# Kernel tuning notes

Measured on AMD Instinct MI355X. Metric: run time of the kernel, lower is better.

## Reference

```python
import jax, jax.numpy as jnp
import numpy as np

N = 8192
D = 512
INSTANCES = 8  # samples per class (balanced PK batch)
ALPHA = 40.0
BASE = 0.5
BIG = 1e9  # finite sentinel instead of inf (safe under vjp)


def setup_inputs() -> dict:
    key = jax.random.key(0)
    emb = jax.random.normal(key, (N, D), dtype=jnp.float32)
    emb = emb / jnp.linalg.norm(emb, axis=1, keepdims=True)  # unit-norm embeddings
    label = jnp.arange(N, dtype=jnp.int64) // INSTANCES       # balanced classes
    return {"embedding": emb, "label": label}


def reference(embedding, label):
    n = embedding.shape[0]
    sim = embedding @ embedding.T                      # [n, n]
    same = label[:, None] == label[None, :]
    eye = jnp.eye(n, dtype=bool)
    pos_mask = same & ~eye                             # positives, excl. self
    neg_mask = ~same                                   # negatives

    # per-row hard-mining thresholds (sampling_method == 1)
    max_pos = jnp.max(jnp.where(pos_mask, sim, -BIG), axis=1)  # pos_pair_[-1]
    min_neg = jnp.min(jnp.where(neg_mask, sim, BIG), axis=1)   # neg_pair_[0]

    neg_sel = neg_mask & (sim < max_pos[:, None])
    pos_sel = pos_mask & (sim > min_neg[:, None])

    pos_cnt = jnp.sum(pos_sel, axis=1)
    neg_cnt = jnp.sum(neg_sel, axis=1)

    # pos_loss_i = mean(1 - pos_pair) if any selected else 0
    pos_sum = jnp.sum(jnp.where(pos_sel, 1.0 - sim, 0.0), axis=1)
    pos_loss = jnp.where(pos_cnt > 0, pos_sum / jnp.maximum(pos_cnt, 1), 0.0)

    # neg_loss_i = (2/alpha)*log(1 + sum exp(alpha*(neg_pair - base))) + mean(neg_pair)
    exp_sum = jnp.sum(jnp.where(neg_sel, jnp.exp(ALPHA * (sim - BASE)), 0.0), axis=1)
    neg_mean = jnp.sum(jnp.where(neg_sel, sim, 0.0), axis=1) / jnp.maximum(neg_cnt, 1)
    neg_loss = jnp.where(neg_cnt > 0, (2.0 / ALPHA) * jnp.log1p(exp_sum) + neg_mean, 0.0)

    loss = jnp.sum(pos_loss + neg_loss) / n
    triplets = jnp.sum(neg_cnt // 2)                   # self.triplets accumulator
    return loss, triplets, 0
```

## Files before the change

kernel.cpp:

```cpp
#include <hip/hip_runtime.h>

typedef float f32x4 __attribute__((ext_vector_type(4)));
typedef short s16x8 __attribute__((ext_vector_type(8)));

#define NROWS 8192
#define DIM   512
#define ALPHA 40.0f
#define BASEV 0.5f
#define BIGF  1e9f
#define NPANEL 64
#define NPAIRS 2080
#define NSLOT  64

#define OFF_HI   0ull
#define OFF_LO   (OFF_HI + (unsigned long long)NROWS*DIM*2)
#define OFF_MAXP (OFF_LO + (unsigned long long)NROWS*DIM*2)
#define OFF_SBLK (OFF_MAXP + (unsigned long long)NROWS*4)
#define OFF_PMIN (OFF_SBLK + 1024ull*64*4)
#define OFF_PCNT (OFF_PMIN + (unsigned long long)NSLOT*NROWS*4)
#define OFF_PSUM (OFF_PCNT + (unsigned long long)NSLOT*NROWS*4)
#define OFF_PEXP (OFF_PSUM + (unsigned long long)NSLOT*NROWS*4)
#define OFF_RLOSS (OFF_PEXP + (unsigned long long)NSLOT*NROWS*4)
#define OFF_RTRIP (OFF_RLOSS + (unsigned long long)NROWS*4)

__device__ inline unsigned short bf16rne(float x) {
    unsigned u = __float_as_uint(x);
    unsigned r = (u + 0x7FFFu + ((u >> 16) & 1u)) >> 16;
    return (unsigned short)r;
}
__device__ inline unsigned pack2(float a, float b) {
    return (unsigned)bf16rne(a) | ((unsigned)bf16rne(b) << 16);
}

__global__ __launch_bounds__(256) void k_prep(const float* __restrict__ emb,
                                              uint4* __restrict__ hi, uint4* __restrict__ lo) {
    __shared__ uint4 lhi[2048];
    __shared__ uint4 llo[2048];
    uint2* lhi2 = (uint2*)lhi;
    uint2* llo2 = (uint2*)llo;

    int t = threadIdx.x;
    int r0 = blockIdx.x * 32;
    const float4* src = (const float4*)(emb + (size_t)r0 * DIM);

#pragma unroll
    for (int i = 0; i < 16; ++i) {
        int f4 = t + i * 256;
        float4 v = src[f4];
        int localrow = f4 >> 7;
        int chunk = (f4 & 127) >> 1;
        int half = f4 & 1;
        int di = (chunk * 32 + localrow) * 2 + half;
        float h0 = __uint_as_float(((unsigned)bf16rne(v.x)) << 16);
        float h1 = __uint_as_float(((unsigned)bf16rne(v.y)) << 16);
        float h2 = __uint_as_float(((unsigned)bf16rne(v.z)) << 16);
        float h3 = __uint_as_float(((unsigned)bf16rne(v.w)) << 16);
        lhi2[di] = (uint2){pack2(v.x, v.y), pack2(v.z, v.w)};
        llo2[di] = (uint2){pack2(v.x - h0, v.y - h1), pack2(v.z - h2, v.w - h3)};
    }
    __syncthreads();
#pragma unroll
    for (int j = 0; j < 8; ++j) {
        int flat = t + j * 256;
        int chunk = flat >> 5, localrow = flat & 31;
        size_t gi = (size_t)chunk * NROWS + r0 + localrow;
        hi[gi] = lhi[flat];
        lo[gi] = llo[flat];
    }
}

__global__ __launch_bounds__(64) void k_gram(const float* __restrict__ emb,
                                             float* __restrict__ simblk,
                                             float* __restrict__ maxpos) {
    __shared__ float A[8 * 516];
    int cls = blockIdx.x, t = threadIdx.x;
    const float* base = emb + (size_t)cls * 8 * DIM;
    for (int it = 0; it < 64; ++it) {
        int idx = t + 64 * it;
        int r = idx >> 9, k = idx & 511;
        A[r * 516 + k] = base[idx];
    }
    __syncthreads();
    int i = t >> 3, j = t & 7;
    const float* ai = A + i * 516;
    const float* aj = A + j * 516;
    float s = 0.f;
    for (int k = 0; k < 512; ++k) s += ai[k] * aj[k];
    simblk[cls * 64 + t] = s;
    float m = (i == j) ? -BIGF : s;
#pragma unroll
    for (int off = 1; off < 8; off <<= 1) m = fmaxf(m, __shfl_xor(m, off, 64));
    if (j == 0) maxpos[cls * 8 + i] = m;
}

#define LD4(d0, d1, d2, d3, base)                                          \
    asm volatile("global_load_dwordx4 %0, %4, off\n\t"                     \
                 "global_load_dwordx4 %1, %4, off offset:256\n\t"          \
                 "global_load_dwordx4 %2, %4, off offset:512\n\t"          \
                 "global_load_dwordx4 %3, %4, off offset:768"              \
                 : "=&v"(d0), "=&v"(d1), "=&v"(d2), "=&v"(d3)              \
                 : "v"(base) : "memory")

#define WAITV(n)                                                           \
    do {                                                                   \
        asm volatile("s_waitcnt vmcnt(" #n ")" ::: "memory");              \
        __builtin_amdgcn_sched_barrier(0);                                 \
    } while (0)

__global__ __launch_bounds__(256, 2) void k_main(const unsigned short* __restrict__ ehi,
                                                 const unsigned short* __restrict__ elo,
                                                 const float* __restrict__ maxpos,
                                                 float* __restrict__ pmin,
                                                 unsigned* __restrict__ pcnt,
                                                 float* __restrict__ psum,
                                                 float* __restrict__ pexp) {
    __shared__ float sMaxA[128], sMaxB[128];
    __shared__ float rMin[2][128];
    __shared__ unsigned rCnt[2][128];
    __shared__ float rSum[2][128], rExp[2][128];
    __shared__ float cMin[2][128];
    __shared__ unsigned cCnt[2][128];
    __shared__ float cSum[2][128], cExp[2][128];

    int t = threadIdx.x;
    int lane = t & 63;
    int w = t >> 6;
    int wr = w >> 1, wc = w & 1;

    int bid = blockIdx.x;
    int wg = (bid & 7) * 260 + (bid >> 3);
    int J = (int)((sqrtf(8.0f * (float)wg + 1.0f) - 1.0f) * 0.5f);
    while ((J + 1) * (J + 2) / 2 <= wg) ++J;
    while (J * (J + 1) / 2 > wg) --J;
    int I = wg - J * (J + 1) / 2;
    int r0 = I * 128, c0 = J * 128;
    bool diag = (I == J);

    if (t < 128) sMaxA[t] = maxpos[r0 + t];
    else sMaxB[t - 128] = maxpos[c0 + (t - 128)];

    int rl = (lane >> 4) * 4;
    int ri = lane & 15;
    int cg = lane >> 4;

    int arow = r0 + wr * 64 + ri;
    int brow = c0 + wc * 64 + ri;
    const char* baseAh = (const char*)((const s16x8*)ehi + (size_t)cg * NROWS + arow);
    const char* baseAl = (const char*)((const s16x8*)elo + (size_t)cg * NROWS + arow);
    const char* baseBh = (const char*)((const s16x8*)ehi + (size_t)cg * NROWS + brow);
    const char* baseBl = (const char*)((const s16x8*)elo + (size_t)cg * NROWS + brow);
    const size_t KSTEP = (size_t)4 * NROWS * 16;

    f32x4 acc[4][4];
#pragma unroll
    for (int m = 0; m < 4; ++m)
#pragma unroll
        for (int n = 0; n < 4; ++n) acc[m][n] = (f32x4){0.f, 0.f, 0.f, 0.f};

    s16x8 aH0[4], aL0[4], bH0[4], bL0[4];
    s16x8 aH1[4], aL1[4], bH1[4], bL1[4];

#define ISSUE0(kt)                                                          \
    do {                                                                    \
        size_t o = (size_t)(kt)*KSTEP;                                      \
        LD4(aH0[0], aH0[1], aH0[2], aH0[3], baseAh + o);                    \
        LD4(aL0[0], aL0[1], aL0[2], aL0[3], baseAl + o);                    \
        LD4(bH0[0], bH0[1], bH0[2], bH0[3], baseBh + o);                    \
        LD4(bL0[0], bL0[1], bL0[2], bL0[3], baseBl + o);                    \
    } while (0)
#define ISSUE1(kt)                                                          \
    do {                                                                    \
        size_t o = (size_t)(kt)*KSTEP;                                      \
        LD4(aH1[0], aH1[1], aH1[2], aH1[3], baseAh + o);                    \
        LD4(aL1[0], aL1[1], aL1[2], aL1[3], baseAl + o);                    \
        LD4(bH1[0], bH1[1], bH1[2], bH1[3], baseBh + o);                    \
        LD4(bL1[0], bL1[1], bL1[2], bL1[3], baseBl + o);                    \
    } while (0)
#define MFMASET(aH, aL, bH, bL)                                             \
    do {                                                                    \
        __builtin_amdgcn_s_setprio(1);                                      \
        _Pragma("unroll") for (int m = 0; m < 4; ++m)                       \
            _Pragma("unroll") for (int n = 0; n < 4; ++n) {                 \
                acc[m][n] = __builtin_amdgcn_mfma_f32_16x16x32_bf16(aH[m], bH[n], acc[m][n], 0, 0, 0); \
                acc[m][n] = __builtin_amdgcn_mfma_f32_16x16x32_bf16(aH[m], bL[n], acc[m][n], 0, 0, 0); \
                acc[m][n] = __builtin_amdgcn_mfma_f32_16x16x32_bf16(aL[m], bH[n], acc[m][n], 0, 0, 0); \
            }                                                               \
        __builtin_amdgcn_s_setprio(0);                                      \
    } while (0)

    ISSUE0(0);
    ISSUE1(1);
#pragma unroll
    for (int kt = 0; kt < 16; kt += 2) {
        WAITV(16);
        MFMASET(aH0, aL0, bH0, bL0);
        __builtin_amdgcn_sched_barrier(0);
        if (kt + 2 < 16) {
            ISSUE0(kt + 2);
            WAITV(16);
        } else {
            WAITV(0);
        }
        MFMASET(aH1, aL1, bH1, bL1);
        __builtin_amdgcn_sched_barrier(0);
        if (kt + 3 < 16) ISSUE1(kt + 3);
    }

    __syncthreads();

    float mxB[4];
#pragma unroll
    for (int n = 0; n < 4; ++n) mxB[n] = sMaxB[wc * 64 + n * 16 + ri];

    float cmn[4], csm[4], ces[4];
    int cct[4];
#pragma unroll
    for (int n = 0; n < 4; ++n) { cmn[n] = BIGF; csm[n] = 0.f; ces[n] = 0.f; cct[n] = 0; }

#pragma unroll
    for (int m = 0; m < 4; ++m) {
#pragma unroll
        for (int jj = 0; jj < 4; ++jj) {
            int lr0 = wr * 64 + m * 16 + rl + jj;
            int grow = r0 + lr0;
            int rcls = grow >> 3;
            float mxA = sMaxA[lr0];
            float mn = BIGF, sm = 0.f, es = 0.f;
            int ct = 0;
#pragma unroll
            for (int n = 0; n < 4; ++n) {
                float v = acc[m][n][jj];
                int gcol = c0 + wc * 64 + n * 16 + ri;
                if ((gcol >> 3) != rcls) {
                    float e = __expf(ALPHA * (v - BASEV));
                    mn = fminf(mn, v);
                    if (v < mxA) { ct++; sm += v; es += e; }
                    if (!diag) {
                        cmn[n] = fminf(cmn[n], v);
                        if (v < mxB[n]) { cct[n]++; csm[n] += v; ces[n] += e; }
                    }
                }
            }
#pragma unroll
            for (int off = 1; off < 16; off <<= 1) {
                mn = fminf(mn, __shfl_xor(mn, off, 64));
                sm += __shfl_xor(sm, off, 64);
                es += __shfl_xor(es, off, 64);
                ct += __shfl_xor(ct, off, 64);
            }
            if ((lane & 15) == 0) {
                rMin[wc][lr0] = mn;
                rCnt[wc][lr0] = (unsigned)ct;
                rSum[wc][lr0] = sm;
                rExp[wc][lr0] = es;
            }
        }
    }

    if (!diag) {
#pragma unroll
        for (int n = 0; n < 4; ++n) {
#pragma unroll
            for (int off = 16; off < 64; off <<= 1) {
                cmn[n] = fminf(cmn[n], __shfl_xor(cmn[n], off, 64));
                csm[n] += __shfl_xor(csm[n], off, 64);
                ces[n] += __shfl_xor(ces[n], off, 64);
                cct[n] += __shfl_xor(cct[n], off, 64);
            }
        }
        if (lane < 16) {
#pragma unroll
            for (int n = 0; n < 4; ++n) {
                int lc = wc * 64 + n * 16 + ri;
                cMin[wr][lc] = cmn[n];
                cCnt[wr][lc] = (unsigned)cct[n];
                cSum[wr][lc] = csm[n];
                cExp[wr][lc] = ces[n];
            }
        }
    }

    __syncthreads();
    if (t < 128) {
        int gi = J * NROWS + r0 + t;
        pmin[gi] = fminf(rMin[0][t], rMin[1][t]);
        pcnt[gi] = rCnt[0][t] + rCnt[1][t];
        psum[gi] = rSum[0][t] + rSum[1][t];
        pexp[gi] = rExp[0][t] + rExp[1][t];
    } else if (!diag) {
        int tc = t - 128;
        int gi = I * NROWS + c0 + tc;
        pmin[gi] = fminf(cMin[0][tc], cMin[1][tc]);
        pcnt[gi] = cCnt[0][tc] + cCnt[1][tc];
        psum[gi] = cSum[0][tc] + cSum[1][tc];
        pexp[gi] = cExp[0][tc] + cExp[1][tc];
    }
}

__global__ __launch_bounds__(256) void k_fin1(const float* __restrict__ pmin,
                                              const unsigned* __restrict__ pcnt,
                                              const float* __restrict__ psum,
                                              const float* __restrict__ pexp,
                                              const float* __restrict__ simblk,
                                              float* __restrict__ rowloss,
                                              unsigned* __restrict__ rowtrip) {
    int row = blockIdx.x * 256 + threadIdx.x;
    float mn = BIGF;
    unsigned ct = 0;
    float sm = 0.f, es = 0.f;
#pragma unroll 8
    for (int c = 0; c < NSLOT; ++c) {
        int gi = c * NROWS + row;
        mn = fminf(mn, pmin[gi]);
        ct += pcnt[gi];
        sm += psum[gi];
        es += pexp[gi];
    }
    int cls = row >> 3, ir = row & 7;
    const float* sb = simblk + cls * 64 + ir * 8;
    float psumv = 0.f;
    int pcntv = 0;
#pragma unroll
    for (int j = 0; j < 8; ++j) {
        if (j == ir) continue;
        float s = sb[j];
        if (s > mn) { pcntv++; psumv += 1.f - s; }
    }
    float pl = (pcntv > 0) ? psumv / (float)pcntv : 0.f;
    float nl = (ct > 0) ? (2.0f / ALPHA) * log1pf(es) + sm / (float)ct : 0.f;
    rowloss[row] = pl + nl;
    rowtrip[row] = ct >> 1;
}

__global__ __launch_bounds__(256) void k_fin2(const float* __restrict__ rowloss,
                                              const unsigned* __restrict__ rowtrip,
                                              float* __restrict__ out) {
    __shared__ float lsum[256];
    __shared__ unsigned long long ltrip[256];
    int t = threadIdx.x;
    float acc = 0.f;
    unsigned long long trip = 0ull;
    for (int it = 0; it < NROWS / 256; ++it) {
        int row = t + it * 256;
        acc += rowloss[row];
        trip += (unsigned long long)rowtrip[row];
    }
    lsum[t] = acc;
    ltrip[t] = trip;
    __syncthreads();
    for (int s = 128; s > 0; s >>= 1) {
        if (t < s) { lsum[t] += lsum[t + s]; ltrip[t] += ltrip[t + s]; }
        __syncthreads();
    }
    if (t == 0) {
        out[0] = lsum[0] / (float)NROWS;
        out[1] = (float)ltrip[0];
        out[2] = 0.f;
    }
}

extern "C" void kernel_launch(void* const* d_in, const int* in_sizes, int n_in,
                              void* d_out, int out_size, void* d_ws, size_t ws_size,
                              hipStream_t stream) {
    const float* emb = (const float*)d_in[0];
    char* ws = (char*)d_ws;
    unsigned short* ehi = (unsigned short*)(ws + OFF_HI);
    unsigned short* elo = (unsigned short*)(ws + OFF_LO);
    float* maxpos = (float*)(ws + OFF_MAXP);
    float* simblk = (float*)(ws + OFF_SBLK);
    float* pmin = (float*)(ws + OFF_PMIN);
    unsigned* pcnt = (unsigned*)(ws + OFF_PCNT);
    float* psum = (float*)(ws + OFF_PSUM);
    float* pexp = (float*)(ws + OFF_PEXP);
    float* rowloss = (float*)(ws + OFF_RLOSS);
    unsigned* rowtrip = (unsigned*)(ws + OFF_RTRIP);
    float* out = (float*)d_out;

    hipLaunchKernelGGL(k_prep, dim3(NROWS / 32), dim3(256), 0, stream,
                       emb, (uint4*)ehi, (uint4*)elo);
    hipLaunchKernelGGL(k_gram, dim3(1024), dim3(64), 0, stream, emb, simblk, maxpos);
    hipLaunchKernelGGL(k_main, dim3(NPAIRS), dim3(256), 0, stream,
                       ehi, elo, maxpos, pmin, pcnt, psum, pexp);
    hipLaunchKernelGGL(k_fin1, dim3(NROWS / 256), dim3(256), 0, stream,
                       pmin, pcnt, psum, pexp, simblk, rowloss, rowtrip);
    hipLaunchKernelGGL(k_fin2, dim3(1), dim3(256), 0, stream, rowloss, rowtrip, out);
}
```

Baseline: 155.1 us.

## Deepen global-load prefetch for A operands to three buffers in MFMA loop

Replaces the two-stage double-buffered register prefetch with a hand-unrolled schedule. It uses three buffers for the A operands and two for the B operands, so the A loads for step k+2 are in flight while step k runs its MFMAs. The vmcnt waits are adjusted to match the deeper pipeline. This is meant to hide more global-load latency, but it raises VGPR pressure and may reduce occupancy.

```diff
diff --git a/kernel.cpp b/kernel.cpp
--- a/kernel.cpp
+++ b/kernel.cpp
@@ -157,24 +157,20 @@
 #pragma unroll
         for (int n = 0; n < 4; ++n) acc[m][n] = (f32x4){0.f, 0.f, 0.f, 0.f};
 
-    s16x8 aH0[4], aL0[4], bH0[4], bL0[4];
-    s16x8 aH1[4], aL1[4], bH1[4], bL1[4];
-
-#define ISSUE0(kt)                                                          \
+    s16x8 aH_0[4], aL_0[4], aH_1[4], aL_1[4], aH_2[4], aL_2[4];
+    s16x8 bH_0[4], bL_0[4], bH_1[4], bL_1[4];
+
+#define ISSUEA(kt, i)                                                       \
     do {                                                                    \
         size_t o = (size_t)(kt)*KSTEP;                                      \
-        LD4(aH0[0], aH0[1], aH0[2], aH0[3], baseAh + o);                    \
-        LD4(aL0[0], aL0[1], aL0[2], aL0[3], baseAl + o);                    \
-        LD4(bH0[0], bH0[1], bH0[2], bH0[3], baseBh + o);                    \
-        LD4(bL0[0], bL0[1], bL0[2], bL0[3], baseBl + o);                    \
+        LD4(aH_##i[0], aH_##i[1], aH_##i[2], aH_##i[3], baseAh + o);        \
+        LD4(aL_##i[0], aL_##i[1], aL_##i[2], aL_##i[3], baseAl + o);        \
     } while (0)
-#define ISSUE1(kt)                                                          \
+#define ISSUEB(kt, i)                                                       \
     do {                                                                    \
         size_t o = (size_t)(kt)*KSTEP;                                      \
-        LD4(aH1[0], aH1[1], aH1[2], aH1[3], baseAh + o);                    \
-        LD4(aL1[0], aL1[1], aL1[2], aL1[3], baseAl + o);                    \
-        LD4(bH1[0], bH1[1], bH1[2], bH1[3], baseBh + o);                    \
-        LD4(bL1[0], bL1[1], bL1[2], bL1[3], baseBl + o);                    \
+        LD4(bH_##i[0], bH_##i[1], bH_##i[2], bH_##i[3], baseBh + o);        \
+        LD4(bL_##i[0], bL_##i[1], bL_##i[2], bL_##i[3], baseBl + o);        \
     } while (0)
 #define MFMASET(aH, aL, bH, bL)                                             \
     do {                                                                    \
@@ -187,24 +183,29 @@
             }                                                               \
         __builtin_amdgcn_s_setprio(0);                                      \
     } while (0)
-
-    ISSUE0(0);
-    ISSUE1(1);
-#pragma unroll
-    for (int kt = 0; kt < 16; kt += 2) {
-        WAITV(16);
-        MFMASET(aH0, aL0, bH0, bL0);
-        __builtin_amdgcn_sched_barrier(0);
-        if (kt + 2 < 16) {
-            ISSUE0(kt + 2);
-            WAITV(16);
-        } else {
-            WAITV(0);
-        }
-        MFMASET(aH1, aL1, bH1, bL1);
-        __builtin_amdgcn_sched_barrier(0);
-        if (kt + 3 < 16) ISSUE1(kt + 3);
-    }
+#define STEP3(ab, bb, wn)                                                   \
+    WAITV(wn);                                                              \
+    MFMASET(aH_##ab, aL_##ab, bH_##bb, bL_##bb);                            \
+    __builtin_amdgcn_sched_barrier(0)
+
+    ISSUEA(0, 0); ISSUEB(0, 0); ISSUEA(1, 1); ISSUEB(1, 1); ISSUEA(2, 2);
+
+    STEP3(0, 0, 24); ISSUEB(2, 0);  ISSUEA(3, 0);
+    STEP3(1, 1, 24); ISSUEB(3, 1);  ISSUEA(4, 1);
+    STEP3(2, 0, 24); ISSUEB(4, 0);  ISSUEA(5, 2);
+    STEP3(0, 1, 24); ISSUEB(5, 1);  ISSUEA(6, 0);
+    STEP3(1, 0, 24); ISSUEB(6, 0);  ISSUEA(7, 1);
+    STEP3(2, 1, 24); ISSUEB(7, 1);  ISSUEA(8, 2);
+    STEP3(0, 0, 24); ISSUEB(8, 0);  ISSUEA(9, 0);
+    STEP3(1, 1, 24); ISSUEB(9, 1);  ISSUEA(10, 1);
+    STEP3(2, 0, 24); ISSUEB(10, 0); ISSUEA(11, 2);
+    STEP3(0, 1, 24); ISSUEB(11, 1); ISSUEA(12, 0);
+    STEP3(1, 0, 24); ISSUEB(12, 0); ISSUEA(13, 1);
+    STEP3(2, 1, 24); ISSUEB(13, 1); ISSUEA(14, 2);
+    STEP3(0, 0, 24); ISSUEB(14, 0); ISSUEA(15, 0);
+    STEP3(1, 1, 24); ISSUEB(15, 1);
+    STEP3(2, 0, 16);
+    STEP3(0, 1, 0);
 
     __syncthreads();
 
```

Result: slower. 161.2 us (+3.9%).
